# Optimization experiments

Hardware: AMD Instinct MI355X
Metric: run time of the kernel (lower is better)

## Reference

```python
import jax, jax.numpy as jnp
import numpy as np

C = 10000   # crystals
K = 5       # elements per crystal
N = C * K   # nodes
EMB = 200   # element embedding length
F = 64      # elem_fea_len
L = 3       # n_graph
H = 3       # heads
HID = 256   # gate/msg hidden dim


def setup_inputs() -> dict:
    key = jax.random.key(0)
    ks = jax.random.split(key, 16)
    # structured intra-crystal all-pairs edge lists (grouped by crystal)
    i_loc = np.repeat(np.arange(K), K)
    j_loc = np.tile(np.arange(K), K)
    base = np.arange(C)[:, None] * K
    self_idx = (base + i_loc).ravel().astype(np.int32)   # [M]
    nbr_idx = (base + j_loc).ravel().astype(np.int32)    # [M]
    cry_idx = np.repeat(np.arange(C), K).astype(np.int32)  # [N]
    def nrm(k, shape, s=0.05):
        return jax.random.normal(k, shape, jnp.float32) * s
    return dict(
        elem_weights=jax.random.uniform(ks[0], (N, 1), jnp.float32, 0.05, 1.0),
        elem_fea=jax.random.normal(ks[1], (N, EMB), jnp.float32),
        self_fea_idx=jnp.asarray(self_idx),
        nbr_fea_idx=jnp.asarray(nbr_idx),
        cry_elem_idx=jnp.asarray(cry_idx),
        n_crystals=C,
        emb_W=nrm(ks[2], (EMB, F - 1)), emb_b=jnp.zeros((F - 1,), jnp.float32),
        g_gate_W1=nrm(ks[3], (L, H, 2 * F, HID)), g_gate_b1=jnp.zeros((L, H, HID), jnp.float32),
        g_gate_W2=nrm(ks[4], (L, H, HID, 1)), g_gate_b2=jnp.zeros((L, H, 1), jnp.float32),
        g_msg_W1=nrm(ks[5], (L, H, 2 * F, HID)), g_msg_b1=jnp.zeros((L, H, HID), jnp.float32),
        g_msg_W2=nrm(ks[6], (L, H, HID, F)), g_msg_b2=jnp.zeros((L, H, F), jnp.float32),
        g_pow=jax.random.normal(ks[7], (L, H), jnp.float32),
        c_gate_W1=nrm(ks[8], (H, F, HID)), c_gate_b1=jnp.zeros((H, HID), jnp.float32),
        c_gate_W2=nrm(ks[9], (H, HID, 1)), c_gate_b2=jnp.zeros((H, 1), jnp.float32),
        c_msg_W1=nrm(ks[10], (H, F, HID)), c_msg_b1=jnp.zeros((H, HID), jnp.float32),
        c_msg_W2=nrm(ks[11], (H, HID, F)), c_msg_b2=jnp.zeros((H, F), jnp.float32),
        c_pow=jax.random.normal(ks[12], (H,), jnp.float32),
    )


def _simple(h, W1, b1, W2, b2):
    # SimpleNetwork: Linear -> LeakyReLU -> Linear (one hidden layer, slope 0.01)
    return jax.nn.leaky_relu(h @ W1 + b1, 0.01) @ W2 + b2


def _attn(fea, weights, index, nseg, gW1, gb1, gW2, gb2, mW1, mb1, mW2, mb2, p):
    # WeightedAttention: segment softmax with learned power on weights
    gate = _simple(fea, gW1, gb1, gW2, gb2)                                   # [E,1]
    gate = gate - jax.ops.segment_max(gate, index, num_segments=nseg)[index]
    gate = weights ** p * jnp.exp(gate)
    gate = gate / (jax.ops.segment_sum(gate, index, num_segments=nseg)[index] + 1e-10)
    msg = _simple(fea, mW1, mb1, mW2, mb2)                                    # [E,F]
    return jax.ops.segment_sum(gate * msg, index, num_segments=nseg)          # [nseg,F]


_attn_heads = jax.vmap(_attn, in_axes=(None, None, None, None, 0, 0, 0, 0, 0, 0, 0, 0, 0))


def _forward(elem_weights, elem_fea, self_fea_idx, nbr_fea_idx, cry_elem_idx, n_crystals,
             emb_W, emb_b,
             g_gate_W1, g_gate_b1, g_gate_W2, g_gate_b2,
             g_msg_W1, g_msg_b1, g_msg_W2, g_msg_b2, g_pow,
             c_gate_W1, c_gate_b1, c_gate_W2, c_gate_b2,
             c_msg_W1, c_msg_b1, c_msg_W2, c_msg_b2, c_pow):
    n_nodes = elem_fea.shape[0]
    x = jnp.concatenate([elem_fea @ emb_W + emb_b, elem_weights], axis=1)     # [N,F]
    w_nbr = elem_weights[nbr_fea_idx]                                          # [M,1]
    for l in range(g_pow.shape[0]):  # n_graph message layers
        cat = jnp.concatenate([x[self_fea_idx], x[nbr_fea_idx]], axis=1)      # [M,2F]
        heads = _attn_heads(cat, w_nbr, self_fea_idx, n_nodes,
                            g_gate_W1[l], g_gate_b1[l], g_gate_W2[l], g_gate_b2[l],
                            g_msg_W1[l], g_msg_b1[l], g_msg_W2[l], g_msg_b2[l], g_pow[l])
        x = heads.mean(0) + x
    heads = _attn_heads(x, elem_weights, cry_elem_idx, n_crystals,
                        c_gate_W1, c_gate_b1, c_gate_W2, c_gate_b2,
                        c_msg_W1, c_msg_b1, c_msg_W2, c_msg_b2, c_pow)
    return heads.mean(0)                                                       # [C,F]


def reference(elem_weights, elem_fea, self_fea_idx, nbr_fea_idx, cry_elem_idx, n_crystals,
              emb_W, emb_b,
              g_gate_W1, g_gate_b1, g_gate_W2, g_gate_b2,
              g_msg_W1, g_msg_b1, g_msg_W2, g_msg_b2, g_pow,
              c_gate_W1, c_gate_b1, c_gate_W2, c_gate_b2,
              c_msg_W1, c_msg_b1, c_msg_W2, c_msg_b2, c_pow):
    return _forward(elem_weights, elem_fea, self_fea_idx, nbr_fea_idx, cry_elem_idx, n_crystals,
                    emb_W, emb_b,
                    g_gate_W1, g_gate_b1, g_gate_W2, g_gate_b2,
                    g_msg_W1, g_msg_b1, g_msg_W2, g_msg_b2, g_pow,
                    c_gate_W1, c_gate_b1, c_gate_W2, c_gate_b2,
                    c_msg_W1, c_msg_b1, c_msg_W2, c_msg_b2, c_pow)
```

## Files before the change

### kernel.cpp

```cpp
#include <hip/hip_runtime.h>
#include <hip/hip_bf16.h>

#define K 5
#define F 64
#define EMBD 200
#define HID 256
#define NH 3
#define NL 3
#define CB 8
#define NB (CB * K)

#define CW 3
#define NWN (CW * K)
#define EWE (CW * K * K)
#define ET 5

typedef _Float16 half8 __attribute__((ext_vector_type(8)));
typedef _Float16 h2 __attribute__((ext_vector_type(2)));
typedef _Float16 h4 __attribute__((ext_vector_type(4)));
typedef __fp16 fp16x2 __attribute__((ext_vector_type(2)));
typedef float f32x4 __attribute__((ext_vector_type(4)));

__device__ __forceinline__ float lrelu(float v) { return v >= 0.f ? v : 0.01f * v; }

__device__ __forceinline__ h2 cvt_pk(float a, float b) {
    union { fp16x2 f; h2 h; } u;
    u.f = __builtin_amdgcn_cvt_pkrtz(a, b);
    return u.h;
}

__device__ __forceinline__ half8 lrelu8(half8 t) {
    half8 z = 0;
    half8 p = __builtin_elementwise_max(t, z);
    half8 n = __builtin_elementwise_min(t, z);
    return p + n * (_Float16)0.01f;
}

#define W1SW_ELEMS 589824
#define W2SW_ELEMS 147456
#define CW1_ELEMS   98304
#define CW2_ELEMS   49152
#define WALL_ELEMS (W1SW_ELEMS + W2SW_ELEMS + CW1_ELEMS + CW2_ELEMS)

#define W1L_ELEMS 196608
#define W2L_ELEMS 49152

__global__ __launch_bounds__(256)
void prep_all(const float* __restrict__ gW1, const float* __restrict__ mW1,
              const float* __restrict__ mW2,
              const float* __restrict__ cgW1, const float* __restrict__ cmW1,
              const float* __restrict__ cmW2,
              _Float16* __restrict__ Wall)
{
    int tid = blockIdx.x * 256 + threadIdx.x;
    if (tid >= WALL_ELEMS) return;
    float v;
    if (tid < W1SW_ELEMS) {
        int j = tid & 7, lane = (tid >> 3) & 63;
        int r1 = tid >> 9;
        int ks = r1 & 1, nt = (r1 >> 1) & 3, chunk = (r1 >> 3) & 3;
        int half = (r1 >> 5) & 1, net = (r1 >> 6) & 1, lh = r1 >> 7;
        int q = lane >> 4, n16 = lane & 15;
        const float* src = net ? mW1 : gW1;
        v = src[((size_t)lh * 128 + half * 64 + ks * 32 + q * 8 + j) * 256
                + chunk * 64 + nt * 16 + n16];
    } else if (tid < W1SW_ELEMS + W2SW_ELEMS) {
        int t2 = tid - W1SW_ELEMS;
        int j = t2 & 7, lane = (t2 >> 3) & 63;
        int r1 = t2 >> 9;
        int nt = r1 & 3, ks2 = (r1 >> 2) & 7, lh = r1 >> 5;
        int q = lane >> 4, n16 = lane & 15;
        v = mW2[((size_t)lh * 256 + ks2 * 32 + q * 8 + j) * 64 + nt * 16 + n16];
    } else if (tid < W1SW_ELEMS + W2SW_ELEMS + CW1_ELEMS) {
        int t2 = tid - (W1SW_ELEMS + W2SW_ELEMS);
        int j = t2 & 7, lane = (t2 >> 3) & 63;
        int r1 = t2 >> 9;
        int ks = r1 & 1, nt = (r1 >> 1) & 3, chunk = (r1 >> 3) & 3;
        int net = (r1 >> 5) & 1, h = r1 >> 6;
        int q = lane >> 4, n16 = lane & 15;
        const float* src = net ? cmW1 : cgW1;
        v = src[((size_t)h * 64 + ks * 32 + q * 8 + j) * 256
                + chunk * 64 + nt * 16 + n16];
    } else {
        int t2 = tid - (W1SW_ELEMS + W2SW_ELEMS + CW1_ELEMS);
        int j = t2 & 7, lane = (t2 >> 3) & 63;
        int r1 = t2 >> 9;
        int nt = r1 & 3, ks2 = (r1 >> 2) & 7, h = r1 >> 5;
        int q = lane >> 4, n16 = lane & 15;
        v = cmW2[((size_t)h * 256 + ks2 * 32 + q * 8 + j) * 64 + nt * 16 + n16];
    }
    Wall[tid] = (_Float16)v;
}

__global__ __launch_bounds__(256)
void prep_layer(const float* __restrict__ gW1, const float* __restrict__ mW1,
                const float* __restrict__ mW2,
                _Float16* __restrict__ W1sw, _Float16* __restrict__ W2sw, int l)
{
    int tid = blockIdx.x * 256 + threadIdx.x;
    if (tid < W1L_ELEMS) {
        int j = tid & 7, lane = (tid >> 3) & 63;
        int r1 = tid >> 9;
        int ks = r1 & 1, nt = (r1 >> 1) & 3, chunk = (r1 >> 3) & 3;
        int half = (r1 >> 5) & 1, net = (r1 >> 6) & 1, hh = r1 >> 7;
        int q = lane >> 4, n16 = lane & 15;
        const float* src = net ? mW1 : gW1;
        float v = src[((size_t)(l * NH + hh) * 128 + half * 64 + ks * 32 + q * 8 + j) * 256
                      + chunk * 64 + nt * 16 + n16];
        W1sw[tid] = (_Float16)v;
    } else {
        int t2 = tid - W1L_ELEMS;
        if (t2 < W2L_ELEMS) {
            int j = t2 & 7, lane = (t2 >> 3) & 63;
            int r1 = t2 >> 9;
            int nt = r1 & 3, ks2 = (r1 >> 2) & 7, hh = r1 >> 5;
            int q = lane >> 4, n16 = lane & 15;
            float v = mW2[((size_t)(l * NH + hh) * 256 + ks2 * 32 + q * 8 + j) * 64
                          + nt * 16 + n16];
            W2sw[t2] = (_Float16)v;
        }
    }
}

__global__ __launch_bounds__(64)
void embed_kernel(const float* __restrict__ fea, const float* __restrict__ W,
                  const float* __restrict__ b, const float* __restrict__ wts,
                  float* __restrict__ x)
{
    int n = blockIdx.x;
    int o = threadIdx.x;
    __shared__ float fs[EMBD];
    for (int e = o; e < EMBD; e += 64) fs[e] = fea[n * EMBD + e];
    __syncthreads();
    if (o < F - 1) {
        float acc = b[o];
#pragma unroll 8
        for (int e = 0; e < EMBD; ++e) acc += fs[e] * W[e * (F - 1) + o];
        x[n * F + o] = acc;
    } else {
        x[n * F + F - 1] = wts[n];
    }
}

#define WAVE_LDS 12288

__global__ __launch_bounds__(256, 2)
void layer_wave(float* __restrict__ x,
                const _Float16* __restrict__ W1sw,
                const _Float16* __restrict__ W2sw,
                const float* __restrict__ gb1, const float* __restrict__ gb2v,
                const float* __restrict__ mb1, const float* __restrict__ mb2,
                const float* __restrict__ gW2, const float* __restrict__ gpw,
                const float* __restrict__ wts, int l, int lhw0, int Ntot)
{
    __shared__ __align__(16) char smem[4 * WAVE_LDS];

    const int t = threadIdx.x, w = t >> 6, lane = t & 63;
    const int q = lane >> 4, m16 = lane & 15;

    char* wb = smem + w * WAVE_LDS;
    _Float16 (*PQ)[16][72] = (_Float16 (*)[16][72])wb;
    _Float16 (*msgL)[72]   = (_Float16 (*)[72])wb;
    float* gateS  = (float*)(wb + 11520);
    float* anormS = (float*)(wb + 11840);
    float* wpowS  = (float*)(wb + 12160);

    const int nw0 = (blockIdx.x * 12 + w * CW) * K;
    const int vn  = (Ntot - nw0 < NWN) ? (Ntot - nw0) : NWN;

    half8 A[2];
    {
        int arow = nw0 + m16;
        if (arow > Ntot - 1) arow = Ntot - 1;
        if (arow < 0) arow = 0;
        const float* xr = x + (size_t)arow * F;
#pragma unroll
        for (int ks = 0; ks < 2; ++ks) {
            float4 f0 = *(const float4*)(xr + ks * 32 + q * 8);
            float4 f1 = *(const float4*)(xr + ks * 32 + q * 8 + 4);
            half8 a;
            a[0] = (_Float16)f0.x; a[1] = (_Float16)f0.y;
            a[2] = (_Float16)f0.z; a[3] = (_Float16)f0.w;
            a[4] = (_Float16)f1.x; a[5] = (_Float16)f1.y;
            a[6] = (_Float16)f1.z; a[7] = (_Float16)f1.w;
            A[ks] = a;
        }
    }

    int iR[ET], jR[ET];
#pragma unroll
    for (int et = 0; et < ET; ++et) {
        int e = et * 16 + m16;
        if (e < EWE) {
            int cl = e / 25, rm = e % 25;
            iR[et] = cl * K + rm / K;
            jR[et] = cl * K + rm % K;
        } else { iR[et] = 15; jR[et] = 15; }
    }

    float oacc[NWN];
#pragma unroll
    for (int n = 0; n < NWN; ++n) oacc[n] = 0.f;

    for (int h = 0; h < NH; ++h) {
        const int lh = l * NH + h, lhw = lhw0 + h;

        if (lane < NWN) {
            int wi = nw0 + lane;
            if (wi > Ntot - 1) wi = Ntot - 1;
            if (wi < 0) wi = 0;
            wpowS[lane] = powf(wts[wi], gpw[lh]);
        }
        if (lane >= NWN && lane < NWN + 5) anormS[EWE + (lane - NWN)] = 0.f;

        f32x4 acc2[ET][4];
#pragma unroll
        for (int et = 0; et < ET; ++et)
#pragma unroll
            for (int nt = 0; nt < 4; ++nt) acc2[et][nt] = (f32x4){0.f, 0.f, 0.f, 0.f};
        float gacc[ET] = {0.f, 0.f, 0.f, 0.f, 0.f};

        for (int c = 0; c < 4; ++c) {
            half8 B2[8];
            {
                const _Float16* W2b = W2sw + ((size_t)lhw * 8 + c * 2) * 2048;
#pragma unroll
                for (int f = 0; f < 8; ++f)
                    B2[f] = *(const half8*)(W2b + ((size_t)f * 64 + lane) * 8);
            }

#pragma unroll
            for (int hf = 0; hf < 4; ++hf) {
                f32x4 accS[4];
#pragma unroll
                for (int nt = 0; nt < 4; ++nt) accS[nt] = (f32x4){0.f, 0.f, 0.f, 0.f};
                const _Float16* Wb = W1sw + ((size_t)lhw * 4 + hf) * 16384 + c * 4096;
#pragma unroll
                for (int nt = 0; nt < 4; ++nt)
#pragma unroll
                    for (int ks = 0; ks < 2; ++ks) {
                        half8 B = *(const half8*)(Wb + ((nt * 2 + ks) * 64 + lane) * 8);
                        accS[nt] = __builtin_amdgcn_mfma_f32_16x16x32_f16(
                            B, A[ks], accS[nt], 0, 0, 0);
                    }
#pragma unroll
                for (int nt = 0; nt < 4; ++nt) {
                    h2 lo = cvt_pk(accS[nt][0], accS[nt][1]);
                    h2 hi = cvt_pk(accS[nt][2], accS[nt][3]);
                    h4 pk = __builtin_shufflevector(lo, hi, 0, 1, 2, 3);
                    *(h4*)&PQ[hf][m16][nt * 16 + q * 4] = pk;
                }
            }

            half8 bg8[2], bm8[2];
            h2 wgh2[2][4];
#pragma unroll
            for (int ks = 0; ks < 2; ++ks) {
                const int ub = c * 64 + ks * 32 + q * 8;
                float4 g0 = *(const float4*)(gb1 + (size_t)lh * HID + ub);
                float4 g1 = *(const float4*)(gb1 + (size_t)lh * HID + ub + 4);
                float4 m0 = *(const float4*)(mb1 + (size_t)lh * HID + ub);
                float4 m1 = *(const float4*)(mb1 + (size_t)lh * HID + ub + 4);
                float4 w0 = *(const float4*)(gW2 + (size_t)lh * HID + ub);
                float4 w1 = *(const float4*)(gW2 + (size_t)lh * HID + ub + 4);
                half8 bg, bm;
                bg[0]=(_Float16)g0.x; bg[1]=(_Float16)g0.y; bg[2]=(_Float16)g0.z; bg[3]=(_Float16)g0.w;
                bg[4]=(_Float16)g1.x; bg[5]=(_Float16)g1.y; bg[6]=(_Float16)g1.z; bg[7]=(_Float16)g1.w;
                bm[0]=(_Float16)m0.x; bm[1]=(_Float16)m0.y; bm[2]=(_Float16)m0.z; bm[3]=(_Float16)m0.w;
                bm[4]=(_Float16)m1.x; bm[5]=(_Float16)m1.y; bm[6]=(_Float16)m1.z; bm[7]=(_Float16)m1.w;
                bg8[ks] = bg; bm8[ks] = bm;
                wgh2[ks][0] = cvt_pk(w0.x, w0.y);
                wgh2[ks][1] = cvt_pk(w0.z, w0.w);
                wgh2[ks][2] = cvt_pk(w1.x, w1.y);
                wgh2[ks][3] = cvt_pk(w1.z, w1.w);
            }

#pragma unroll
            for (int et = 0; et < ET; ++et) {
                half8 af[2];
#pragma unroll
                for (int ks = 0; ks < 2; ++ks) {
                    const int ub = ks * 32 + q * 8;
                    half8 pg = *(const half8*)&PQ[0][iR[et]][ub];
                    half8 qg = *(const half8*)&PQ[1][jR[et]][ub];
                    half8 pm = *(const half8*)&PQ[2][iR[et]][ub];
                    half8 qm = *(const half8*)&PQ[3][jR[et]][ub];
                    half8 tg = lrelu8(pg + qg + bg8[ks]);
                    h2 t01 = __builtin_shufflevector(tg, tg, 0, 1);
                    h2 t23 = __builtin_shufflevector(tg, tg, 2, 3);
                    h2 t45 = __builtin_shufflevector(tg, tg, 4, 5);
                    h2 t67 = __builtin_shufflevector(tg, tg, 6, 7);
                    gacc[et] = __builtin_amdgcn_fdot2(t01, wgh2[ks][0], gacc[et], false);
                    gacc[et] = __builtin_amdgcn_fdot2(t23, wgh2[ks][1], gacc[et], false);
                    gacc[et] = __builtin_amdgcn_fdot2(t45, wgh2[ks][2], gacc[et], false);
                    gacc[et] = __builtin_amdgcn_fdot2(t67, wgh2[ks][3], gacc[et], false);
                    af[ks] = lrelu8(pm + qm + bm8[ks]);
                }
#pragma unroll
                for (int nt = 0; nt < 4; ++nt)
#pragma unroll
                    for (int ks = 0; ks < 2; ++ks)
                        acc2[et][nt] = __builtin_amdgcn_mfma_f32_16x16x32_f16(
                            af[ks], B2[ks * 4 + nt], acc2[et][nt], 0, 0, 0);
            }
        }

        const float gb2s = gb2v[lh];
#pragma unroll
        for (int et = 0; et < ET; ++et) {
            float g = gacc[et];
            g += __shfl_xor(g, 16);
            g += __shfl_xor(g, 32);
            if (q == 0) gateS[et * 16 + m16] = g + gb2s;
        }

        if (lane < NWN) {
            const int cl5 = (lane / K) * K;
            float gg[K], mx = -1e30f;
#pragma unroll
            for (int jj = 0; jj < K; ++jj) {
                gg[jj] = gateS[lane * K + jj];
                mx = fmaxf(mx, gg[jj]);
            }
            float s = 0.f, wv[K];
#pragma unroll
            for (int jj = 0; jj < K; ++jj) {
                wv[jj] = wpowS[cl5 + jj] * expf(gg[jj] - mx);
                s += wv[jj];
            }
            float inv = 1.f / (s + 1e-10f) * (1.f / 3.f);
#pragma unroll
            for (int jj = 0; jj < K; ++jj) anormS[lane * K + jj] = wv[jj] * inv;
        }

        float b2v[4];
#pragma unroll
        for (int nt = 0; nt < 4; ++nt) b2v[nt] = mb2[(size_t)lh * F + nt * 16 + m16];
#pragma unroll
        for (int et = 0; et < ET; ++et) {
            f32x4 an = *(const f32x4*)&anormS[et * 16 + q * 4];
#pragma unroll
            for (int nt = 0; nt < 4; ++nt)
#pragma unroll
                for (int rg = 0; rg < 4; ++rg) {
                    float v = (acc2[et][nt][rg] + b2v[nt]) * an[rg];
                    msgL[et * 16 + q * 4 + rg][nt * 16 + m16] = (_Float16)v;
                }
        }

#pragma unroll
        for (int n = 0; n < NWN; ++n) {
            float s = 0.f;
#pragma unroll
            for (int jj = 0; jj < K; ++jj) s += (float)msgL[n * K + jj][lane];
            oacc[n] += s;
        }
    }

#pragma unroll
    for (int n = 0; n < NWN; ++n) {
        if (n < vn) {
            size_t idx = (size_t)(nw0 + n) * F + lane;
            x[idx] = oacc[n] + x[idx];
        }
    }
}

#define PWAVE_LDS 4800

__global__ __launch_bounds__(256, 2)
void pool_wave(const float* __restrict__ x,
               const _Float16* __restrict__ cW1sw,
               const _Float16* __restrict__ cW2sw,
               const float* __restrict__ cgb1, const float* __restrict__ cgb2v,
               const float* __restrict__ cmb1, const float* __restrict__ cmb2,
               const float* __restrict__ cgW2, const float* __restrict__ cpw,
               const float* __restrict__ wts, float* __restrict__ out, int Ctot)
{
    __shared__ __align__(16) char smem[4 * PWAVE_LDS];

    const int t = threadIdx.x, w = t >> 6, lane = t & 63;
    const int q = lane >> 4, m16 = lane & 15;

    char* wb = smem + w * PWAVE_LDS;
    _Float16 (*PQ)[16][72] = (_Float16 (*)[16][72])wb;
    _Float16 (*msgL)[72]   = (_Float16 (*)[72])wb;
    float* gateS  = (float*)(wb + 4608);
    float* anormS = (float*)(wb + 4672);
    float* wpowS  = (float*)(wb + 4736);

    const int c0  = blockIdx.x * 12 + w * CW;
    const int nw0 = c0 * K;
    const int Ntot = Ctot * K;
    const int vc  = (Ctot - c0 < CW) ? (Ctot - c0) : CW;

    half8 A[2];
    {
        int arow = nw0 + m16;
        if (arow > Ntot - 1) arow = Ntot - 1;
        if (arow < 0) arow = 0;
        const float* xr = x + (size_t)arow * F;
#pragma unroll
        for (int ks = 0; ks < 2; ++ks) {
            float4 f0 = *(const float4*)(xr + ks * 32 + q * 8);
            float4 f1 = *(const float4*)(xr + ks * 32 + q * 8 + 4);
            half8 a;
            a[0] = (_Float16)f0.x; a[1] = (_Float16)f0.y;
            a[2] = (_Float16)f0.z; a[3] = (_Float16)f0.w;
            a[4] = (_Float16)f1.x; a[5] = (_Float16)f1.y;
            a[6] = (_Float16)f1.z; a[7] = (_Float16)f1.w;
            A[ks] = a;
        }
    }

    float oacc[CW] = {0.f, 0.f, 0.f};

    for (int h = 0; h < NH; ++h) {
        if (lane < NWN) {
            int wi = nw0 + lane;
            if (wi > Ntot - 1) wi = Ntot - 1;
            if (wi < 0) wi = 0;
            wpowS[lane] = powf(wts[wi], cpw[h]);
        }
        if (lane == NWN) anormS[15] = 0.f;

        f32x4 acc2[4];
#pragma unroll
        for (int nt = 0; nt < 4; ++nt) acc2[nt] = (f32x4){0.f, 0.f, 0.f, 0.f};
        float gacc = 0.f;

        for (int c = 0; c < 4; ++c) {
            half8 B2[8];
            {
                const _Float16* W2b = cW2sw + (size_t)h * 16384 + c * 4096;
#pragma unroll
                for (int f = 0; f < 8; ++f)
                    B2[f] = *(const half8*)(W2b + ((size_t)f * 64 + lane) * 8);
            }

#pragma unroll
            for (int net = 0; net < 2; ++net) {
                f32x4 accS[4];
#pragma unroll
                for (int nt = 0; nt < 4; ++nt) accS[nt] = (f32x4){0.f, 0.f, 0.f, 0.f};
                const _Float16* Wb = cW1sw + ((size_t)(h * 2 + net) * 4 + c) * 4096;
#pragma unroll
                for (int nt = 0; nt < 4; ++nt)
#pragma unroll
                    for (int ks = 0; ks < 2; ++ks) {
                        half8 B = *(const half8*)(Wb + ((nt * 2 + ks) * 64 + lane) * 8);
                        accS[nt] = __builtin_amdgcn_mfma_f32_16x16x32_f16(
                            B, A[ks], accS[nt], 0, 0, 0);
                    }
#pragma unroll
                for (int nt = 0; nt < 4; ++nt) {
                    h2 lo = cvt_pk(accS[nt][0], accS[nt][1]);
                    h2 hi = cvt_pk(accS[nt][2], accS[nt][3]);
                    h4 pk = __builtin_shufflevector(lo, hi, 0, 1, 2, 3);
                    *(h4*)&PQ[net][m16][nt * 16 + q * 4] = pk;
                }
            }

            half8 bg8[2], bm8[2];
            h2 wgh2[2][4];
#pragma unroll
            for (int ks = 0; ks < 2; ++ks) {
                const int ub = c * 64 + ks * 32 + q * 8;
                float4 g0 = *(const float4*)(cgb1 + (size_t)h * HID + ub);
                float4 g1 = *(const float4*)(cgb1 + (size_t)h * HID + ub + 4);
                float4 m0 = *(const float4*)(cmb1 + (size_t)h * HID + ub);
                float4 m1 = *(const float4*)(cmb1 + (size_t)h * HID + ub + 4);
                float4 w0 = *(const float4*)(cgW2 + (size_t)h * HID + ub);
                float4 w1 = *(const float4*)(cgW2 + (size_t)h * HID + ub + 4);
                half8 bg, bm;
                bg[0]=(_Float16)g0.x; bg[1]=(_Float16)g0.y; bg[2]=(_Float16)g0.z; bg[3]=(_Float16)g0.w;
                bg[4]=(_Float16)g1.x; bg[5]=(_Float16)g1.y; bg[6]=(_Float16)g1.z; bg[7]=(_Float16)g1.w;
                bm[0]=(_Float16)m0.x; bm[1]=(_Float16)m0.y; bm[2]=(_Float16)m0.z; bm[3]=(_Float16)m0.w;
                bm[4]=(_Float16)m1.x; bm[5]=(_Float16)m1.y; bm[6]=(_Float16)m1.z; bm[7]=(_Float16)m1.w;
                bg8[ks] = bg; bm8[ks] = bm;
                wgh2[ks][0] = cvt_pk(w0.x, w0.y);
                wgh2[ks][1] = cvt_pk(w0.z, w0.w);
                wgh2[ks][2] = cvt_pk(w1.x, w1.y);
                wgh2[ks][3] = cvt_pk(w1.z, w1.w);
            }

            {
                half8 af[2];
#pragma unroll
                for (int ks = 0; ks < 2; ++ks) {
                    const int ub = ks * 32 + q * 8;
                    half8 pg = *(const half8*)&PQ[0][m16][ub];
                    half8 pm = *(const half8*)&PQ[1][m16][ub];
                    half8 tg = lrelu8(pg + bg8[ks]);
                    h2 t01 = __builtin_shufflevector(tg, tg, 0, 1);
                    h2 t23 = __builtin_shufflevector(tg, tg, 2, 3);
                    h2 t45 = __builtin_shufflevector(tg, tg, 4, 5);
                    h2 t67 = __builtin_shufflevector(tg, tg, 6, 7);
                    gacc = __builtin_amdgcn_fdot2(t01, wgh2[ks][0], gacc, false);
                    gacc = __builtin_amdgcn_fdot2(t23, wgh2[ks][1], gacc, false);
                    gacc = __builtin_amdgcn_fdot2(t45, wgh2[ks][2], gacc, false);
                    gacc = __builtin_amdgcn_fdot2(t67, wgh2[ks][3], gacc, false);
                    af[ks] = lrelu8(pm + bm8[ks]);
                }
#pragma unroll
                for (int nt = 0; nt < 4; ++nt)
#pragma unroll
                    for (int ks = 0; ks < 2; ++ks)
                        acc2[nt] = __builtin_amdgcn_mfma_f32_16x16x32_f16(
                            af[ks], B2[ks * 4 + nt], acc2[nt], 0, 0, 0);
            }
        }

        const float gb2s = cgb2v[h];
        {
            float g = gacc;
            g += __shfl_xor(g, 16);
            g += __shfl_xor(g, 32);
            if (q == 0) gateS[m16] = g + gb2s;
        }

        if (lane < CW) {
            const int n0 = lane * K;
            float gg[K], mx = -1e30f;
#pragma unroll
            for (int jj = 0; jj < K; ++jj) {
                gg[jj] = gateS[n0 + jj];
                mx = fmaxf(mx, gg[jj]);
            }
            float s = 0.f, wv[K];
#pragma unroll
            for (int jj = 0; jj < K; ++jj) {
                wv[jj] = wpowS[n0 + jj] * expf(gg[jj] - mx);
                s += wv[jj];
            }
            float inv = 1.f / (s + 1e-10f) * (1.f / 3.f);
#pragma unroll
            for (int jj = 0; jj < K; ++jj) anormS[n0 + jj] = wv[jj] * inv;
        }

        float b2v[4];
#pragma unroll
        for (int nt = 0; nt < 4; ++nt) b2v[nt] = cmb2[(size_t)h * F + nt * 16 + m16];
#pragma unroll
        for (int nt = 0; nt < 4; ++nt)
#pragma unroll
            for (int rg = 0; rg < 4; ++rg) {
                int row = q * 4 + rg;
                float v = (acc2[nt][rg] + b2v[nt]) * anormS[row];
                msgL[row][nt * 16 + m16] = (_Float16)v;
            }

#pragma unroll
        for (int cl = 0; cl < CW; ++cl) {
            float s = 0.f;
#pragma unroll
            for (int jj = 0; jj < K; ++jj) s += (float)msgL[cl * K + jj][lane];
            oacc[cl] += s;
        }
    }

#pragma unroll
    for (int cl = 0; cl < CW; ++cl)
        if (cl < vc)
            out[(size_t)(c0 + cl) * F + lane] = oacc[cl];
}

__global__ __launch_bounds__(256)
void pool_kernel(const float* __restrict__ x,
                 const float* __restrict__ cgW1, const float* __restrict__ cgb1,
                 const float* __restrict__ cgW2, const float* __restrict__ cgb2,
                 const float* __restrict__ cmW1, const float* __restrict__ cmb1,
                 const float* __restrict__ cmW2, const float* __restrict__ cmb2,
                 const float* __restrict__ cpw, const float* __restrict__ wts,
                 float* __restrict__ out)
{
    __shared__ float xs[K * F];
    __shared__ float hmS[K][HID];
    __shared__ float msgS[K][F];
    __shared__ float outacc[F];
    __shared__ float b1g[HID], b1m[HID], w2g[HID];
    __shared__ float b2mS[F];
    __shared__ float gpart[K][2];
    __shared__ float gate_s[K];
    __shared__ float anorm[K];
    __shared__ float wn[K], wpow[K];

    const int c = blockIdx.x;
    const int t = threadIdx.x;
    const int wave = t >> 6, lane = t & 63;

    for (int d = t; d < K * F; d += 256) xs[d] = x[c * K * F + d];
    if (t < F) outacc[t] = 0.f;
    if (t < K) wn[t] = wts[c * K + t];
    __syncthreads();

    for (int h = 0; h < NH; ++h) {
        if (t < HID) {
            b1g[t] = cgb1[(size_t)h * HID + t];
            b1m[t] = cmb1[(size_t)h * HID + t];
            w2g[t] = cgW2[(size_t)h * HID + t];
        }
        if (t < F) b2mS[t] = cmb2[(size_t)h * F + t];
        if (t < K) wpow[t] = powf(wn[t], cpw[h]);
        __syncthreads();

        {
            const int grp = t >> 7;
            const int up  = t & 127;
            const float* Wb = (grp == 0 ? cgW1 : cmW1) + (size_t)h * F * HID;
            const float2* W2p = (const float2*)Wb;
            float acc[K][2];
#pragma unroll
            for (int i = 0; i < K; ++i) { acc[i][0] = 0.f; acc[i][1] = 0.f; }
            for (int k = 0; k < F; ++k) {
                float2 wv = W2p[k * (HID / 2) + up];
#pragma unroll
                for (int i = 0; i < K; ++i) {
                    float xv = xs[i * F + k];
                    acc[i][0] += xv * wv.x;
                    acc[i][1] += xv * wv.y;
                }
            }
            if (grp == 0) {
#pragma unroll
                for (int i = 0; i < K; ++i) {
                    float h0 = lrelu(acc[i][0] + b1g[2 * up]);
                    float h1 = lrelu(acc[i][1] + b1g[2 * up + 1]);
                    float part = h0 * w2g[2 * up] + h1 * w2g[2 * up + 1];
#pragma unroll
                    for (int s = 32; s; s >>= 1) part += __shfl_xor(part, s);
                    if (lane == 0) gpart[i][wave & 1] = part;
                }
            } else {
#pragma unroll
                for (int i = 0; i < K; ++i) {
                    hmS[i][2 * up]     = lrelu(acc[i][0] + b1m[2 * up]);
                    hmS[i][2 * up + 1] = lrelu(acc[i][1] + b1m[2 * up + 1]);
                }
            }
        }
        __syncthreads();
        if (t < K) gate_s[t] = cgb2[h] + gpart[t][0] + gpart[t][1];

        {
            const float2* W232 = (const float2*)(cmW2 + (size_t)h * HID * F);
            if (t < K * (F / 2)) {
                int i  = t >> 5;
                int op = t & 31;
                float a0 = b2mS[2 * op], a1 = b2mS[2 * op + 1];
#pragma unroll 8
                for (int u = 0; u < HID; ++u) {
                    float2 wv = W232[u * (F / 2) + op];
                    float hv = hmS[i][u];
                    a0 += hv * wv.x;
                    a1 += hv * wv.y;
                }
                msgS[i][2 * op]     = a0;
                msgS[i][2 * op + 1] = a1;
            }
        }
        __syncthreads();

        if (t == 0) {
            float mx = -1e30f;
#pragma unroll
            for (int i = 0; i < K; ++i) mx = fmaxf(mx, gate_s[i]);
            float wv[K], s = 0.f;
#pragma unroll
            for (int i = 0; i < K; ++i) {
                wv[i] = wpow[i] * expf(gate_s[i] - mx);
                s += wv[i];
            }
            float inv = 1.f / (s + 1e-10f);
#pragma unroll
            for (int i = 0; i < K; ++i) anorm[i] = wv[i] * inv;
        }
        __syncthreads();

        if (t < F) {
            float s = 0.f;
#pragma unroll
            for (int i = 0; i < K; ++i) s += anorm[i] * msgS[i][t];
            outacc[t] += s * (1.f / 3.f);
        }
        __syncthreads();
    }

    if (t < F) out[(size_t)c * F + t] = outacc[t];
}

extern "C" void kernel_launch(void* const* d_in, const int* in_sizes, int n_in,
                              void* d_out, int out_size, void* d_ws, size_t ws_size,
                              hipStream_t stream)
{
    const float* wts  = (const float*)d_in[0];
    const float* fea  = (const float*)d_in[1];
    const float* embW = (const float*)d_in[6];
    const float* embB = (const float*)d_in[7];
    const float* gW1  = (const float*)d_in[8];
    const float* gb1  = (const float*)d_in[9];
    const float* gW2  = (const float*)d_in[10];
    const float* gb2  = (const float*)d_in[11];
    const float* mW1  = (const float*)d_in[12];
    const float* mb1  = (const float*)d_in[13];
    const float* mW2  = (const float*)d_in[14];
    const float* mb2  = (const float*)d_in[15];
    const float* gpw  = (const float*)d_in[16];
    const float* cgW1 = (const float*)d_in[17];
    const float* cgb1 = (const float*)d_in[18];
    const float* cgW2 = (const float*)d_in[19];
    const float* cgb2 = (const float*)d_in[20];
    const float* cmW1 = (const float*)d_in[21];
    const float* cmb1 = (const float*)d_in[22];
    const float* cmW2 = (const float*)d_in[23];
    const float* cmb2 = (const float*)d_in[24];
    const float* cpw  = (const float*)d_in[25];

    const int N = in_sizes[0];
    const int C = N / K;
    const int layer_blocks = (C + 11) / 12;

    float* x = (float*)d_ws;
    const size_t xbytes = (size_t)N * F * 4;
    const size_t need = xbytes + (size_t)WALL_ELEMS * 2;

    embed_kernel<<<N, 64, 0, stream>>>(fea, embW, embB, wts, x);

    if (ws_size >= need) {
        _Float16* Wall  = (_Float16*)((char*)d_ws + xbytes);
        _Float16* W1sw  = Wall;
        _Float16* W2sw  = Wall + W1SW_ELEMS;
        _Float16* cW1sw = Wall + W1SW_ELEMS + W2SW_ELEMS;
        _Float16* cW2sw = Wall + W1SW_ELEMS + W2SW_ELEMS + CW1_ELEMS;

        prep_all<<<(WALL_ELEMS + 255) / 256, 256, 0, stream>>>(
            gW1, mW1, mW2, cgW1, cmW1, cmW2, Wall);
        for (int l = 0; l < NL; ++l)
            layer_wave<<<layer_blocks, 256, 0, stream>>>(x, W1sw, W2sw,
                                                         gb1, gb2, mb1, mb2, gW2, gpw, wts,
                                                         l, l * NH, N);
        pool_wave<<<layer_blocks, 256, 0, stream>>>(x, cW1sw, cW2sw,
                                                    cgb1, cgb2, cmb1, cmb2, cgW2, cpw, wts,
                                                    (float*)d_out, C);
    } else {
        _Float16* W1sw = (_Float16*)d_out;
        _Float16* W2sw = (_Float16*)((char*)d_out + 393216);
        for (int l = 0; l < NL; ++l) {
            prep_layer<<<(W1L_ELEMS + W2L_ELEMS) / 256, 256, 0, stream>>>(
                gW1, mW1, mW2, W1sw, W2sw, l);
            layer_wave<<<layer_blocks, 256, 0, stream>>>(x, W1sw, W2sw,
                                                         gb1, gb2, mb1, mb2, gW2, gpw, wts,
                                                         l, 0, N);
        }
        pool_kernel<<<C, 256, 0, stream>>>(x, cgW1, cgb1, cgW2, cgb2,
                                           cmW1, cmb1, cmW2, cmb2, cpw, wts,
                                           (float*)d_out);
    }
}
```

Baseline: 781.4 us.

## Fuse all graph layers and pooling into a single persistent wave kernel

Replaces the three per-layer layer_wave launches and the pool_wave launch with one net_wave kernel. Each wave keeps its 15 node feature rows in registers across layers and passes the fp16 copy through LDS to rebuild the MFMA A operand, so the intermediate x never goes back to global memory. Crystals never interact across layers, so the fusion is valid without any grid-wide sync. This removes three launch boundaries and the x reload/store traffic per layer, at the cost of higher register pressure (xcur[15] plus the accumulators), which may reduce occupancy or cause spills.

```diff
diff --git a/kernel.cpp b/kernel.cpp
--- a/kernel.cpp
+++ b/kernel.cpp
@@ -7,8 +7,6 @@
 #define HID 256
 #define NH 3
 #define NL 3
-#define CB 8
-#define NB (CB * K)
 
 #define CW 3
 #define NWN (CW * K)
@@ -145,6 +143,407 @@
 #define WAVE_LDS 12288
 
 __global__ __launch_bounds__(256, 2)
+void net_wave(const float* __restrict__ x,
+              const _Float16* __restrict__ W1sw,
+              const _Float16* __restrict__ W2sw,
+              const float* __restrict__ gb1, const float* __restrict__ gb2v,
+              const float* __restrict__ mb1, const float* __restrict__ mb2,
+              const float* __restrict__ gW2, const float* __restrict__ gpw,
+              const _Float16* __restrict__ cW1sw,
+              const _Float16* __restrict__ cW2sw,
+              const float* __restrict__ cgb1, const float* __restrict__ cgb2v,
+              const float* __restrict__ cmb1, const float* __restrict__ cmb2,
+              const float* __restrict__ cgW2, const float* __restrict__ cpw,
+              const float* __restrict__ wts, float* __restrict__ out, int Ntot)
+{
+    __shared__ __align__(16) char smem[4 * WAVE_LDS];
+
+    const int t = threadIdx.x, w = t >> 6, lane = t & 63;
+    const int q = lane >> 4, m16 = lane & 15;
+
+    char* wb = smem + w * WAVE_LDS;
+    _Float16 (*PQ)[16][72] = (_Float16 (*)[16][72])wb;
+    _Float16 (*msgL)[72]   = (_Float16 (*)[72])wb;
+    _Float16 (*xS)[72]     = (_Float16 (*)[72])(wb + 9216);
+    float* gateS  = (float*)(wb + 11520);
+    float* anormS = (float*)(wb + 11840);
+    float* wpowS  = (float*)(wb + 12160);
+
+    const int nw0 = (blockIdx.x * 12 + w * CW) * K;
+    const int c0  = blockIdx.x * 12 + w * CW;
+    const int Ctot = Ntot / K;
+    const int vn  = (Ntot - nw0 < NWN) ? (Ntot - nw0) : NWN;
+    const int vc  = (Ctot - c0 < CW) ? (Ctot - c0) : CW;
+    (void)vn;
+
+    half8 A[2];
+    {
+        int arow = nw0 + m16;
+        if (arow > Ntot - 1) arow = Ntot - 1;
+        if (arow < 0) arow = 0;
+        const float* xr = x + (size_t)arow * F;
+#pragma unroll
+        for (int ks = 0; ks < 2; ++ks) {
+            float4 f0 = *(const float4*)(xr + ks * 32 + q * 8);
+            float4 f1 = *(const float4*)(xr + ks * 32 + q * 8 + 4);
+            half8 a;
+            a[0] = (_Float16)f0.x; a[1] = (_Float16)f0.y;
+            a[2] = (_Float16)f0.z; a[3] = (_Float16)f0.w;
+            a[4] = (_Float16)f1.x; a[5] = (_Float16)f1.y;
+            a[6] = (_Float16)f1.z; a[7] = (_Float16)f1.w;
+            A[ks] = a;
+        }
+    }
+
+    float xcur[NWN];
+#pragma unroll
+    for (int n = 0; n < NWN; ++n) {
+        int r = nw0 + n;
+        if (r > Ntot - 1) r = Ntot - 1;
+        if (r < 0) r = 0;
+        xcur[n] = x[(size_t)r * F + lane];
+    }
+
+    int iR[ET], jR[ET];
+#pragma unroll
+    for (int et = 0; et < ET; ++et) {
+        int e = et * 16 + m16;
+        if (e < EWE) {
+            int cl = e / 25, rm = e % 25;
+            iR[et] = cl * K + rm / K;
+            jR[et] = cl * K + rm % K;
+        } else { iR[et] = 15; jR[et] = 15; }
+    }
+
+#pragma clang loop unroll(disable)
+    for (int l = 0; l < NL; ++l) {
+        float oacc[NWN];
+#pragma unroll
+        for (int n = 0; n < NWN; ++n) oacc[n] = 0.f;
+
+        for (int h = 0; h < NH; ++h) {
+            const int lh = l * NH + h, lhw = lh;
+
+            if (lane < NWN) {
+                int wi = nw0 + lane;
+                if (wi > Ntot - 1) wi = Ntot - 1;
+                if (wi < 0) wi = 0;
+                wpowS[lane] = powf(wts[wi], gpw[lh]);
+            }
+            if (lane >= NWN && lane < NWN + 5) anormS[EWE + (lane - NWN)] = 0.f;
+
+            f32x4 acc2[ET][4];
+#pragma unroll
+            for (int et = 0; et < ET; ++et)
+#pragma unroll
+                for (int nt = 0; nt < 4; ++nt) acc2[et][nt] = (f32x4){0.f, 0.f, 0.f, 0.f};
+            float gacc[ET] = {0.f, 0.f, 0.f, 0.f, 0.f};
+
+            for (int c = 0; c < 4; ++c) {
+                half8 B2[8];
+                {
+                    const _Float16* W2b = W2sw + ((size_t)lhw * 8 + c * 2) * 2048;
+#pragma unroll
+                    for (int f = 0; f < 8; ++f)
+                        B2[f] = *(const half8*)(W2b + ((size_t)f * 64 + lane) * 8);
+                }
+
+#pragma unroll
+                for (int hf = 0; hf < 4; ++hf) {
+                    f32x4 accS[4];
+#pragma unroll
+                    for (int nt = 0; nt < 4; ++nt) accS[nt] = (f32x4){0.f, 0.f, 0.f, 0.f};
+                    const _Float16* Wb = W1sw + ((size_t)lhw * 4 + hf) * 16384 + c * 4096;
+#pragma unroll
+                    for (int nt = 0; nt < 4; ++nt)
+#pragma unroll
+                        for (int ks = 0; ks < 2; ++ks) {
+                            half8 B = *(const half8*)(Wb + ((nt * 2 + ks) * 64 + lane) * 8);
+                            accS[nt] = __builtin_amdgcn_mfma_f32_16x16x32_f16(
+                                B, A[ks], accS[nt], 0, 0, 0);
+                        }
+#pragma unroll
+                    for (int nt = 0; nt < 4; ++nt) {
+                        h2 lo = cvt_pk(accS[nt][0], accS[nt][1]);
+                        h2 hi = cvt_pk(accS[nt][2], accS[nt][3]);
+                        h4 pk = __builtin_shufflevector(lo, hi, 0, 1, 2, 3);
+                        *(h4*)&PQ[hf][m16][nt * 16 + q * 4] = pk;
+                    }
+                }
+
+                half8 bg8[2], bm8[2];
+                h2 wgh2[2][4];
+#pragma unroll
+                for (int ks = 0; ks < 2; ++ks) {
+                    const int ub = c * 64 + ks * 32 + q * 8;
+                    float4 g0 = *(const float4*)(gb1 + (size_t)lh * HID + ub);
+                    float4 g1 = *(const float4*)(gb1 + (size_t)lh * HID + ub + 4);
+                    float4 m0 = *(const float4*)(mb1 + (size_t)lh * HID + ub);
+                    float4 m1 = *(const float4*)(mb1 + (size_t)lh * HID + ub + 4);
+                    float4 w0 = *(const float4*)(gW2 + (size_t)lh * HID + ub);
+                    float4 w1 = *(const float4*)(gW2 + (size_t)lh * HID + ub + 4);
+                    half8 bg, bm;
+                    bg[0]=(_Float16)g0.x; bg[1]=(_Float16)g0.y; bg[2]=(_Float16)g0.z; bg[3]=(_Float16)g0.w;
+                    bg[4]=(_Float16)g1.x; bg[5]=(_Float16)g1.y; bg[6]=(_Float16)g1.z; bg[7]=(_Float16)g1.w;
+                    bm[0]=(_Float16)m0.x; bm[1]=(_Float16)m0.y; bm[2]=(_Float16)m0.z; bm[3]=(_Float16)m0.w;
+                    bm[4]=(_Float16)m1.x; bm[5]=(_Float16)m1.y; bm[6]=(_Float16)m1.z; bm[7]=(_Float16)m1.w;
+                    bg8[ks] = bg; bm8[ks] = bm;
+                    wgh2[ks][0] = cvt_pk(w0.x, w0.y);
+                    wgh2[ks][1] = cvt_pk(w0.z, w0.w);
+                    wgh2[ks][2] = cvt_pk(w1.x, w1.y);
+                    wgh2[ks][3] = cvt_pk(w1.z, w1.w);
+                }
+
+#pragma unroll
+                for (int et = 0; et < ET; ++et) {
+                    half8 af[2];
+#pragma unroll
+                    for (int ks = 0; ks < 2; ++ks) {
+                        const int ub = ks * 32 + q * 8;
+                        half8 pg = *(const half8*)&PQ[0][iR[et]][ub];
+                        half8 qg = *(const half8*)&PQ[1][jR[et]][ub];
+                        half8 pm = *(const half8*)&PQ[2][iR[et]][ub];
+                        half8 qm = *(const half8*)&PQ[3][jR[et]][ub];
+                        half8 tg = lrelu8(pg + qg + bg8[ks]);
+                        h2 t01 = __builtin_shufflevector(tg, tg, 0, 1);
+                        h2 t23 = __builtin_shufflevector(tg, tg, 2, 3);
+                        h2 t45 = __builtin_shufflevector(tg, tg, 4, 5);
+                        h2 t67 = __builtin_shufflevector(tg, tg, 6, 7);
+                        gacc[et] = __builtin_amdgcn_fdot2(t01, wgh2[ks][0], gacc[et], false);
+                        gacc[et] = __builtin_amdgcn_fdot2(t23, wgh2[ks][1], gacc[et], false);
+                        gacc[et] = __builtin_amdgcn_fdot2(t45, wgh2[ks][2], gacc[et], false);
+                        gacc[et] = __builtin_amdgcn_fdot2(t67, wgh2[ks][3], gacc[et], false);
+                        af[ks] = lrelu8(pm + qm + bm8[ks]);
+                    }
+#pragma unroll
+                    for (int nt = 0; nt < 4; ++nt)
+#pragma unroll
+                        for (int ks = 0; ks < 2; ++ks)
+                            acc2[et][nt] = __builtin_amdgcn_mfma_f32_16x16x32_f16(
+                                af[ks], B2[ks * 4 + nt], acc2[et][nt], 0, 0, 0);
+                }
+            }
+
+            const float gb2s = gb2v[lh];
+#pragma unroll
+            for (int et = 0; et < ET; ++et) {
+                float g = gacc[et];
+                g += __shfl_xor(g, 16);
+                g += __shfl_xor(g, 32);
+                if (q == 0) gateS[et * 16 + m16] = g + gb2s;
+            }
+
+            if (lane < NWN) {
+                const int cl5 = (lane / K) * K;
+                float gg[K], mx = -1e30f;
+#pragma unroll
+                for (int jj = 0; jj < K; ++jj) {
+                    gg[jj] = gateS[lane * K + jj];
+                    mx = fmaxf(mx, gg[jj]);
+                }
+                float s = 0.f, wv[K];
+#pragma unroll
+                for (int jj = 0; jj < K; ++jj) {
+                    wv[jj] = wpowS[cl5 + jj] * expf(gg[jj] - mx);
+                    s += wv[jj];
+                }
+                float inv = 1.f / (s + 1e-10f) * (1.f / 3.f);
+#pragma unroll
+                for (int jj = 0; jj < K; ++jj) anormS[lane * K + jj] = wv[jj] * inv;
+            }
+
+            float b2v[4];
+#pragma unroll
+            for (int nt = 0; nt < 4; ++nt) b2v[nt] = mb2[(size_t)lh * F + nt * 16 + m16];
+#pragma unroll
+            for (int et = 0; et < ET; ++et) {
+                f32x4 an = *(const f32x4*)&anormS[et * 16 + q * 4];
+#pragma unroll
+                for (int nt = 0; nt < 4; ++nt)
+#pragma unroll
+                    for (int rg = 0; rg < 4; ++rg) {
+                        float v = (acc2[et][nt][rg] + b2v[nt]) * an[rg];
+                        msgL[et * 16 + q * 4 + rg][nt * 16 + m16] = (_Float16)v;
+                    }
+            }
+
+#pragma unroll
+            for (int n = 0; n < NWN; ++n) {
+                float s = 0.f;
+#pragma unroll
+                for (int jj = 0; jj < K; ++jj) s += (float)msgL[n * K + jj][lane];
+                oacc[n] += s;
+            }
+        }
+
+#pragma unroll
+        for (int n = 0; n < NWN; ++n) {
+            float xn = oacc[n] + xcur[n];
+            xcur[n] = xn;
+            xS[n][lane] = (_Float16)xn;
+        }
+        xS[15][lane] = (_Float16)0.f;
+#pragma unroll
+        for (int ks = 0; ks < 2; ++ks)
+            A[ks] = *(const half8*)&xS[m16][ks * 32 + q * 8];
+    }
+
+    _Float16 (*PQp)[16][72] = (_Float16 (*)[16][72])wb;
+    _Float16 (*msgP)[72]    = (_Float16 (*)[72])wb;
+
+    float oaccP[CW] = {0.f, 0.f, 0.f};
+
+    for (int h = 0; h < NH; ++h) {
+        if (lane < NWN) {
+            int wi = nw0 + lane;
+            if (wi > Ntot - 1) wi = Ntot - 1;
+            if (wi < 0) wi = 0;
+            wpowS[lane] = powf(wts[wi], cpw[h]);
+        }
+        if (lane == NWN) anormS[15] = 0.f;
+
+        f32x4 acc2[4];
+#pragma unroll
+        for (int nt = 0; nt < 4; ++nt) acc2[nt] = (f32x4){0.f, 0.f, 0.f, 0.f};
+        float gacc = 0.f;
+
+        for (int c = 0; c < 4; ++c) {
+            half8 B2[8];
+            {
+                const _Float16* W2b = cW2sw + (size_t)h * 16384 + c * 4096;
+#pragma unroll
+                for (int f = 0; f < 8; ++f)
+                    B2[f] = *(const half8*)(W2b + ((size_t)f * 64 + lane) * 8);
+            }
+
+#pragma unroll
+            for (int net = 0; net < 2; ++net) {
+                f32x4 accS[4];
+#pragma unroll
+                for (int nt = 0; nt < 4; ++nt) accS[nt] = (f32x4){0.f, 0.f, 0.f, 0.f};
+                const _Float16* Wb = cW1sw + ((size_t)(h * 2 + net) * 4 + c) * 4096;
+#pragma unroll
+                for (int nt = 0; nt < 4; ++nt)
+#pragma unroll
+                    for (int ks = 0; ks < 2; ++ks) {
+                        half8 B = *(const half8*)(Wb + ((nt * 2 + ks) * 64 + lane) * 8);
+                        accS[nt] = __builtin_amdgcn_mfma_f32_16x16x32_f16(
+                            B, A[ks], accS[nt], 0, 0, 0);
+                    }
+#pragma unroll
+                for (int nt = 0; nt < 4; ++nt) {
+                    h2 lo = cvt_pk(accS[nt][0], accS[nt][1]);
+                    h2 hi = cvt_pk(accS[nt][2], accS[nt][3]);
+                    h4 pk = __builtin_shufflevector(lo, hi, 0, 1, 2, 3);
+                    *(h4*)&PQp[net][m16][nt * 16 + q * 4] = pk;
+                }
+            }
+
+            half8 bg8[2], bm8[2];
+            h2 wgh2[2][4];
+#pragma unroll
+            for (int ks = 0; ks < 2; ++ks) {
+                const int ub = c * 64 + ks * 32 + q * 8;
+                float4 g0 = *(const float4*)(cgb1 + (size_t)h * HID + ub);
+                float4 g1 = *(const float4*)(cgb1 + (size_t)h * HID + ub + 4);
+                float4 m0 = *(const float4*)(cmb1 + (size_t)h * HID + ub);
+                float4 m1 = *(const float4*)(cmb1 + (size_t)h * HID + ub + 4);
+                float4 w0 = *(const float4*)(cgW2 + (size_t)h * HID + ub);
+                float4 w1 = *(const float4*)(cgW2 + (size_t)h * HID + ub + 4);
+                half8 bg, bm;
+                bg[0]=(_Float16)g0.x; bg[1]=(_Float16)g0.y; bg[2]=(_Float16)g0.z; bg[3]=(_Float16)g0.w;
+                bg[4]=(_Float16)g1.x; bg[5]=(_Float16)g1.y; bg[6]=(_Float16)g1.z; bg[7]=(_Float16)g1.w;
+                bm[0]=(_Float16)m0.x; bm[1]=(_Float16)m0.y; bm[2]=(_Float16)m0.z; bm[3]=(_Float16)m0.w;
+                bm[4]=(_Float16)m1.x; bm[5]=(_Float16)m1.y; bm[6]=(_Float16)m1.z; bm[7]=(_Float16)m1.w;
+                bg8[ks] = bg; bm8[ks] = bm;
+                wgh2[ks][0] = cvt_pk(w0.x, w0.y);
+                wgh2[ks][1] = cvt_pk(w0.z, w0.w);
+                wgh2[ks][2] = cvt_pk(w1.x, w1.y);
+                wgh2[ks][3] = cvt_pk(w1.z, w1.w);
+            }
+
+            {
+                half8 af[2];
+#pragma unroll
+                for (int ks = 0; ks < 2; ++ks) {
+                    const int ub = ks * 32 + q * 8;
+                    half8 pg = *(const half8*)&PQp[0][m16][ub];
+                    half8 pm = *(const half8*)&PQp[1][m16][ub];
+                    half8 tg = lrelu8(pg + bg8[ks]);
+                    h2 t01 = __builtin_shufflevector(tg, tg, 0, 1);
+                    h2 t23 = __builtin_shufflevector(tg, tg, 2, 3);
+                    h2 t45 = __builtin_shufflevector(tg, tg, 4, 5);
+                    h2 t67 = __builtin_shufflevector(tg, tg, 6, 7);
+                    gacc = __builtin_amdgcn_fdot2(t01, wgh2[ks][0], gacc, false);
+                    gacc = __builtin_amdgcn_fdot2(t23, wgh2[ks][1], gacc, false);
+                    gacc = __builtin_amdgcn_fdot2(t45, wgh2[ks][2], gacc, false);
+                    gacc = __builtin_amdgcn_fdot2(t67, wgh2[ks][3], gacc, false);
+                    af[ks] = lrelu8(pm + bm8[ks]);
+                }
+#pragma unroll
+                for (int nt = 0; nt < 4; ++nt)
+#pragma unroll
+                    for (int ks = 0; ks < 2; ++ks)
+                        acc2[nt] = __builtin_amdgcn_mfma_f32_16x16x32_f16(
+                            af[ks], B2[ks * 4 + nt], acc2[nt], 0, 0, 0);
+            }
+        }
+
+        const float gb2s = cgb2v[h];
+        {
+            float g = gacc;
+            g += __shfl_xor(g, 16);
+            g += __shfl_xor(g, 32);
+            if (q == 0) gateS[m16] = g + gb2s;
+        }
+
+        if (lane < CW) {
+            const int n0 = lane * K;
+            float gg[K], mx = -1e30f;
+#pragma unroll
+            for (int jj = 0; jj < K; ++jj) {
+                gg[jj] = gateS[n0 + jj];
+                mx = fmaxf(mx, gg[jj]);
+            }
+            float s = 0.f, wv[K];
+#pragma unroll
+            for (int jj = 0; jj < K; ++jj) {
+                wv[jj] = wpowS[n0 + jj] * expf(gg[jj] - mx);
+                s += wv[jj];
+            }
+            float inv = 1.f / (s + 1e-10f) * (1.f / 3.f);
+#pragma unroll
+            for (int jj = 0; jj < K; ++jj) anormS[n0 + jj] = wv[jj] * inv;
+        }
+
+        float b2v[4];
+#pragma unroll
+        for (int nt = 0; nt < 4; ++nt) b2v[nt] = cmb2[(size_t)h * F + nt * 16 + m16];
+#pragma unroll
+        for (int nt = 0; nt < 4; ++nt)
+#pragma unroll
+            for (int rg = 0; rg < 4; ++rg) {
+                int row = q * 4 + rg;
+                float v = (acc2[nt][rg] + b2v[nt]) * anormS[row];
+                msgP[row][nt * 16 + m16] = (_Float16)v;
+            }
+
+#pragma unroll
+        for (int cl = 0; cl < CW; ++cl) {
+            float s = 0.f;
+#pragma unroll
+            for (int jj = 0; jj < K; ++jj) s += (float)msgP[cl * K + jj][lane];
+            oaccP[cl] += s;
+        }
+    }
+
+#pragma unroll
+    for (int cl = 0; cl < CW; ++cl)
+        if (cl < vc)
+            out[(size_t)(c0 + cl) * F + lane] = oaccP[cl];
+}
+
+__global__ __launch_bounds__(256, 2)
 void layer_wave(float* __restrict__ x,
                 const _Float16* __restrict__ W1sw,
                 const _Float16* __restrict__ W2sw,
@@ -364,205 +763,6 @@
             x[idx] = oacc[n] + x[idx];
         }
     }
-}
-
-#define PWAVE_LDS 4800
-
-__global__ __launch_bounds__(256, 2)
-void pool_wave(const float* __restrict__ x,
-               const _Float16* __restrict__ cW1sw,
-               const _Float16* __restrict__ cW2sw,
-               const float* __restrict__ cgb1, const float* __restrict__ cgb2v,
-               const float* __restrict__ cmb1, const float* __restrict__ cmb2,
-               const float* __restrict__ cgW2, const float* __restrict__ cpw,
-               const float* __restrict__ wts, float* __restrict__ out, int Ctot)
-{
-    __shared__ __align__(16) char smem[4 * PWAVE_LDS];
-
-    const int t = threadIdx.x, w = t >> 6, lane = t & 63;
-    const int q = lane >> 4, m16 = lane & 15;
-
-    char* wb = smem + w * PWAVE_LDS;
-    _Float16 (*PQ)[16][72] = (_Float16 (*)[16][72])wb;
-    _Float16 (*msgL)[72]   = (_Float16 (*)[72])wb;
-    float* gateS  = (float*)(wb + 4608);
-    float* anormS = (float*)(wb + 4672);
-    float* wpowS  = (float*)(wb + 4736);
-
-    const int c0  = blockIdx.x * 12 + w * CW;
-    const int nw0 = c0 * K;
-    const int Ntot = Ctot * K;
-    const int vc  = (Ctot - c0 < CW) ? (Ctot - c0) : CW;
-
-    half8 A[2];
-    {
-        int arow = nw0 + m16;
-        if (arow > Ntot - 1) arow = Ntot - 1;
-        if (arow < 0) arow = 0;
-        const float* xr = x + (size_t)arow * F;
-#pragma unroll
-        for (int ks = 0; ks < 2; ++ks) {
-            float4 f0 = *(const float4*)(xr + ks * 32 + q * 8);
-            float4 f1 = *(const float4*)(xr + ks * 32 + q * 8 + 4);
-            half8 a;
-            a[0] = (_Float16)f0.x; a[1] = (_Float16)f0.y;
-            a[2] = (_Float16)f0.z; a[3] = (_Float16)f0.w;
-            a[4] = (_Float16)f1.x; a[5] = (_Float16)f1.y;
-            a[6] = (_Float16)f1.z; a[7] = (_Float16)f1.w;
-            A[ks] = a;
-        }
-    }
-
-    float oacc[CW] = {0.f, 0.f, 0.f};
-
-    for (int h = 0; h < NH; ++h) {
-        if (lane < NWN) {
-            int wi = nw0 + lane;
-            if (wi > Ntot - 1) wi = Ntot - 1;
-            if (wi < 0) wi = 0;
-            wpowS[lane] = powf(wts[wi], cpw[h]);
-        }
-        if (lane == NWN) anormS[15] = 0.f;
-
-        f32x4 acc2[4];
-#pragma unroll
-        for (int nt = 0; nt < 4; ++nt) acc2[nt] = (f32x4){0.f, 0.f, 0.f, 0.f};
-        float gacc = 0.f;
-
-        for (int c = 0; c < 4; ++c) {
-            half8 B2[8];
-            {
-                const _Float16* W2b = cW2sw + (size_t)h * 16384 + c * 4096;
-#pragma unroll
-                for (int f = 0; f < 8; ++f)
-                    B2[f] = *(const half8*)(W2b + ((size_t)f * 64 + lane) * 8);
-            }
-
-#pragma unroll
-            for (int net = 0; net < 2; ++net) {
-                f32x4 accS[4];
-#pragma unroll
-                for (int nt = 0; nt < 4; ++nt) accS[nt] = (f32x4){0.f, 0.f, 0.f, 0.f};
-                const _Float16* Wb = cW1sw + ((size_t)(h * 2 + net) * 4 + c) * 4096;
-#pragma unroll
-                for (int nt = 0; nt < 4; ++nt)
-#pragma unroll
-                    for (int ks = 0; ks < 2; ++ks) {
-                        half8 B = *(const half8*)(Wb + ((nt * 2 + ks) * 64 + lane) * 8);
-                        accS[nt] = __builtin_amdgcn_mfma_f32_16x16x32_f16(
-                            B, A[ks], accS[nt], 0, 0, 0);
-                    }
-#pragma unroll
-                for (int nt = 0; nt < 4; ++nt) {
-                    h2 lo = cvt_pk(accS[nt][0], accS[nt][1]);
-                    h2 hi = cvt_pk(accS[nt][2], accS[nt][3]);
-                    h4 pk = __builtin_shufflevector(lo, hi, 0, 1, 2, 3);
-                    *(h4*)&PQ[net][m16][nt * 16 + q * 4] = pk;
-                }
-            }
-
-            half8 bg8[2], bm8[2];
-            h2 wgh2[2][4];
-#pragma unroll
-            for (int ks = 0; ks < 2; ++ks) {
-                const int ub = c * 64 + ks * 32 + q * 8;
-                float4 g0 = *(const float4*)(cgb1 + (size_t)h * HID + ub);
-                float4 g1 = *(const float4*)(cgb1 + (size_t)h * HID + ub + 4);
-                float4 m0 = *(const float4*)(cmb1 + (size_t)h * HID + ub);
-                float4 m1 = *(const float4*)(cmb1 + (size_t)h * HID + ub + 4);
-                float4 w0 = *(const float4*)(cgW2 + (size_t)h * HID + ub);
-                float4 w1 = *(const float4*)(cgW2 + (size_t)h * HID + ub + 4);
-                half8 bg, bm;
-                bg[0]=(_Float16)g0.x; bg[1]=(_Float16)g0.y; bg[2]=(_Float16)g0.z; bg[3]=(_Float16)g0.w;
-                bg[4]=(_Float16)g1.x; bg[5]=(_Float16)g1.y; bg[6]=(_Float16)g1.z; bg[7]=(_Float16)g1.w;
-                bm[0]=(_Float16)m0.x; bm[1]=(_Float16)m0.y; bm[2]=(_Float16)m0.z; bm[3]=(_Float16)m0.w;
-                bm[4]=(_Float16)m1.x; bm[5]=(_Float16)m1.y; bm[6]=(_Float16)m1.z; bm[7]=(_Float16)m1.w;
-                bg8[ks] = bg; bm8[ks] = bm;
-                wgh2[ks][0] = cvt_pk(w0.x, w0.y);
-                wgh2[ks][1] = cvt_pk(w0.z, w0.w);
-                wgh2[ks][2] = cvt_pk(w1.x, w1.y);
-                wgh2[ks][3] = cvt_pk(w1.z, w1.w);
-            }
-
-            {
-                half8 af[2];
-#pragma unroll
-                for (int ks = 0; ks < 2; ++ks) {
-                    const int ub = ks * 32 + q * 8;
-                    half8 pg = *(const half8*)&PQ[0][m16][ub];
-                    half8 pm = *(const half8*)&PQ[1][m16][ub];
-                    half8 tg = lrelu8(pg + bg8[ks]);
-                    h2 t01 = __builtin_shufflevector(tg, tg, 0, 1);
-                    h2 t23 = __builtin_shufflevector(tg, tg, 2, 3);
-                    h2 t45 = __builtin_shufflevector(tg, tg, 4, 5);
-                    h2 t67 = __builtin_shufflevector(tg, tg, 6, 7);
-                    gacc = __builtin_amdgcn_fdot2(t01, wgh2[ks][0], gacc, false);
-                    gacc = __builtin_amdgcn_fdot2(t23, wgh2[ks][1], gacc, false);
-                    gacc = __builtin_amdgcn_fdot2(t45, wgh2[ks][2], gacc, false);
-                    gacc = __builtin_amdgcn_fdot2(t67, wgh2[ks][3], gacc, false);
-                    af[ks] = lrelu8(pm + bm8[ks]);
-                }
-#pragma unroll
-                for (int nt = 0; nt < 4; ++nt)
-#pragma unroll
-                    for (int ks = 0; ks < 2; ++ks)
-                        acc2[nt] = __builtin_amdgcn_mfma_f32_16x16x32_f16(
-                            af[ks], B2[ks * 4 + nt], acc2[nt], 0, 0, 0);
-            }
-        }
-
-        const float gb2s = cgb2v[h];
-        {
-            float g = gacc;
-            g += __shfl_xor(g, 16);
-            g += __shfl_xor(g, 32);
-            if (q == 0) gateS[m16] = g + gb2s;
-        }
-
-        if (lane < CW) {
-            const int n0 = lane * K;
-            float gg[K], mx = -1e30f;
-#pragma unroll
-            for (int jj = 0; jj < K; ++jj) {
-                gg[jj] = gateS[n0 + jj];
-                mx = fmaxf(mx, gg[jj]);
-            }
-            float s = 0.f, wv[K];
-#pragma unroll
-            for (int jj = 0; jj < K; ++jj) {
-                wv[jj] = wpowS[n0 + jj] * expf(gg[jj] - mx);
-                s += wv[jj];
-            }
-            float inv = 1.f / (s + 1e-10f) * (1.f / 3.f);
-#pragma unroll
-            for (int jj = 0; jj < K; ++jj) anormS[n0 + jj] = wv[jj] * inv;
-        }
-
-        float b2v[4];
-#pragma unroll
-        for (int nt = 0; nt < 4; ++nt) b2v[nt] = cmb2[(size_t)h * F + nt * 16 + m16];
-#pragma unroll
-        for (int nt = 0; nt < 4; ++nt)
-#pragma unroll
-            for (int rg = 0; rg < 4; ++rg) {
-                int row = q * 4 + rg;
-                float v = (acc2[nt][rg] + b2v[nt]) * anormS[row];
-                msgL[row][nt * 16 + m16] = (_Float16)v;
-            }
-
-#pragma unroll
-        for (int cl = 0; cl < CW; ++cl) {
-            float s = 0.f;
-#pragma unroll
-            for (int jj = 0; jj < K; ++jj) s += (float)msgL[cl * K + jj][lane];
-            oacc[cl] += s;
-        }
-    }
-
-#pragma unroll
-    for (int cl = 0; cl < CW; ++cl)
-        if (cl < vc)
-            out[(size_t)(c0 + cl) * F + lane] = oacc[cl];
 }
 
 __global__ __launch_bounds__(256)
@@ -735,13 +935,10 @@
 
         prep_all<<<(WALL_ELEMS + 255) / 256, 256, 0, stream>>>(
             gW1, mW1, mW2, cgW1, cmW1, cmW2, Wall);
-        for (int l = 0; l < NL; ++l)
-            layer_wave<<<layer_blocks, 256, 0, stream>>>(x, W1sw, W2sw,
-                                                         gb1, gb2, mb1, mb2, gW2, gpw, wts,
-                                                         l, l * NH, N);
-        pool_wave<<<layer_blocks, 256, 0, stream>>>(x, cW1sw, cW2sw,
-                                                    cgb1, cgb2, cmb1, cmb2, cgW2, cpw, wts,
-                                                    (float*)d_out, C);
+        net_wave<<<layer_blocks, 256, 0, stream>>>(
+            x, W1sw, W2sw, gb1, gb2, mb1, mb2, gW2, gpw,
+            cW1sw, cW2sw, cgb1, cgb2, cmb1, cmb2, cgW2, cpw,
+            wts, (float*)d_out, N);
     } else {
         _Float16* W1sw = (_Float16*)d_out;
         _Float16* W2sw = (_Float16*)((char*)d_out + 393216);
```

Measured after the change: 723.1 us. -7.5%, faster.
